# Kernel optimization log

Measured on AMD Instinct MI355X. Metric: run time of the kernel, lower is better.

Reference implementation:

```python
import jax, jax.numpy as jnp
import numpy as np

HIDDEN = 1024
HEADS = 16
HEAD_DIM = HIDDEN // HEADS
POS_DIM = 128
B, S = 2, 2048
ROPE_BASE = 10000.0


def setup_inputs() -> dict:
    key = jax.random.key(0)
    ks = jax.random.split(key, 8)
    sd = 1.0 / np.sqrt(HIDDEN)
    return {
        "x":   jax.random.normal(ks[0], (B, S, HIDDEN), dtype=jnp.float32),
        "W_q": jax.random.normal(ks[1], (HIDDEN, HIDDEN), dtype=jnp.float32) * sd,
        "W_k": jax.random.normal(ks[2], (HIDDEN, HIDDEN), dtype=jnp.float32) * sd,
        "W_v": jax.random.normal(ks[3], (HIDDEN, HIDDEN), dtype=jnp.float32) * sd,
        "W_o": jax.random.normal(ks[4], (HIDDEN, HIDDEN), dtype=jnp.float32) * sd,
        "repo_W1": jax.random.normal(ks[5], (HIDDEN, POS_DIM), dtype=jnp.float32) * sd,
        "repo_b1": jnp.zeros((POS_DIM,), dtype=jnp.float32),
        "repo_W2": jax.random.normal(ks[6], (POS_DIM, 1), dtype=jnp.float32) * (1.0 / np.sqrt(POS_DIM)),
        "repo_b2": jnp.zeros((1,), dtype=jnp.float32),
    }


def _repo_positions(x, W1, b1, W2, b2):
    # 2-layer MLP -> scalar per token; softplus + cumsum gives monotone learned positions
    h = jax.nn.gelu(jnp.einsum("bsd,dp->bsp", x, W1) + b1)
    raw = (jnp.einsum("bsp,po->bso", h, W2) + b2)[..., 0]      # (B, S)
    return jnp.cumsum(jax.nn.softplus(raw), axis=1)             # (B, S)


def _apply_rope(q, k, positions):
    # q, k: (B, S, H, Dh); positions: (B, S) continuous
    half = HEAD_DIM // 2
    inv_freq = 1.0 / (ROPE_BASE ** (jnp.arange(0, HEAD_DIM, 2, dtype=jnp.float32) / HEAD_DIM))
    angles = positions[:, :, None] * inv_freq                   # (B, S, half)
    cos = jnp.cos(angles)[:, :, None, :]                        # (B, S, 1, half)
    sin = jnp.sin(angles)[:, :, None, :]

    def rot(t):
        t1, t2 = t[..., :half], t[..., half:]
        return jnp.concatenate([t1 * cos - t2 * sin, t1 * sin + t2 * cos], axis=-1)

    return rot(q), rot(k)


def reference(x, W_q, W_k, W_v, W_o, repo_W1, repo_b1, repo_W2, repo_b2):
    scale = 1.0 / np.sqrt(HEAD_DIM)
    q = jnp.einsum("bsd,de->bse", x, W_q).reshape(B, S, HEADS, HEAD_DIM)
    k = jnp.einsum("bsd,de->bse", x, W_k).reshape(B, S, HEADS, HEAD_DIM)
    v = jnp.einsum("bsd,de->bse", x, W_v).reshape(B, S, HEADS, HEAD_DIM)

    positions = _repo_positions(x, repo_W1, repo_b1, repo_W2, repo_b2)
    q, k = _apply_rope(q, k, positions)

    # explicit O(S^2) attention, matching the torch module
    scores = jnp.einsum("bqhd,bkhd->bhqk", q, k) * scale        # (B, H, S, S)
    attn = jax.nn.softmax(scores, axis=-1)
    out = jnp.einsum("bhqk,bkhd->bqhd", attn, v)                # (B, S, H, Dh)
    out = out.reshape(B, S, HIDDEN)
    return jnp.einsum("bsd,de->bse", out, W_o)
```

## Files before the change

### kernel.cpp

```cpp
#include <hip/hip_runtime.h>
#include <hip/hip_bf16.h>
#include <math.h>

#define HIDDEN 1024
#define HEADS 16
#define HEAD_DIM 64
#define POS_DIM 128
#define BATCH 2
#define SEQ 2048
#define TOKENS (BATCH * SEQ)

typedef _Float16 f16;
typedef __attribute__((ext_vector_type(8))) _Float16 f16x8;
typedef __attribute__((ext_vector_type(4))) _Float16 f16x4;
typedef __attribute__((ext_vector_type(4))) float f32x4;

__device__ __forceinline__ void glds16(const f16* g, f16* l) {
    __builtin_amdgcn_global_load_lds((const __attribute__((address_space(1))) unsigned int*)g,
                                     (__attribute__((address_space(3))) unsigned int*)l, 16, 0, 0);
}

__global__ __launch_bounds__(256) void cast_x_kernel(const float* __restrict__ x,
                                                     f16* __restrict__ o) {
    const int i = (blockIdx.x * 256 + threadIdx.x) * 8;
    const float4 u = *(const float4*)(x + i);
    const float4 v = *(const float4*)(x + i + 4);
    f16x8 r = {(f16)u.x, (f16)u.y, (f16)u.z, (f16)u.w,
               (f16)v.x, (f16)v.y, (f16)v.z, (f16)v.w};
    *(f16x8*)(o + i) = r;
}

__global__ __launch_bounds__(256) void cast_wt4_kernel(const float* __restrict__ W0,
                                                       const float* __restrict__ W1,
                                                       const float* __restrict__ W2,
                                                       const float* __restrict__ W3,
                                                       f16* __restrict__ Wt) {
    __shared__ float ts[32][33];
    const int t = threadIdx.x;
    const int z = blockIdx.z;
    const float* W = (z == 0) ? W0 : (z == 1) ? W1 : (z == 2) ? W2 : W3;
    f16* dst = Wt + (size_t)z * HIDDEN * HIDDEN;
    const int k0 = blockIdx.y * 32, n0 = blockIdx.x * 32;
    {
        const int r = t >> 3, c4 = (t & 7) * 4;
        const float4 u = *(const float4*)(W + (size_t)(k0 + r) * HIDDEN + n0 + c4);
        ts[r][c4 + 0] = u.x; ts[r][c4 + 1] = u.y; ts[r][c4 + 2] = u.z; ts[r][c4 + 3] = u.w;
    }
    __syncthreads();
    {
        const int r = t >> 3, c4 = (t & 7) * 4;
        f16* o = dst + (size_t)(n0 + r) * HIDDEN + k0 + c4;
        o[0] = (f16)ts[c4 + 0][r]; o[1] = (f16)ts[c4 + 1][r];
        o[2] = (f16)ts[c4 + 2][r]; o[3] = (f16)ts[c4 + 3][r];
    }
}

__global__ __launch_bounds__(256) void cast_w1t_kernel(const float* __restrict__ W1,
                                                       f16* __restrict__ Wh,
                                                       f16* __restrict__ Wl) {
    __shared__ float ts[32][33];
    const int t = threadIdx.x;
    const int k0 = blockIdx.y * 32, p0 = blockIdx.x * 32;
    {
        const int r = t >> 3, c4 = (t & 7) * 4;
        const float4 u = *(const float4*)(W1 + (size_t)(k0 + r) * POS_DIM + p0 + c4);
        ts[r][c4 + 0] = u.x; ts[r][c4 + 1] = u.y; ts[r][c4 + 2] = u.z; ts[r][c4 + 3] = u.w;
    }
    __syncthreads();
    {
        const int r = t >> 3, c4 = (t & 7) * 4;
        f16* oh = Wh + (size_t)(p0 + r) * HIDDEN + k0 + c4;
        f16* ol = Wl + (size_t)(p0 + r) * HIDDEN + k0 + c4;
#pragma unroll
        for (int u = 0; u < 4; ++u) {
            const float v = ts[c4 + u][r];
            const f16 hi = (f16)v;
            oh[u] = hi;
            ol[u] = (f16)(v - (float)hi);
        }
    }
}

__global__ __launch_bounds__(256, 3) void gemm_gll(const f16* __restrict__ A,
                                                   const f16* __restrict__ Bt,
                                                   f16* __restrict__ Cb,
                                                   float* __restrict__ Cf,
                                                   int N, int f16out) {
    __shared__ __align__(16) f16 As[128 * 64];
    __shared__ __align__(16) f16 Bs[128 * 64];
    const int tid = threadIdx.x;
    const int w = tid >> 6, lane = tid & 63;
    const int g = lane >> 4, c = lane & 15;
    const int m0 = blockIdx.y * 128, n0 = blockIdx.x * 128;
    const int wm = (w & 1) * 64, wn = (w >> 1) * 64;

    const int lrow = lane >> 3;
    const int lseg = (lane & 7) ^ lrow;
    const f16* gA = A + (size_t)(m0 + w * 32 + lrow) * 1024 + lseg * 8;
    const f16* gB = Bt + (size_t)(n0 + w * 32 + lrow) * 1024 + lseg * 8;
    f16* lA = &As[(w * 32) * 64];
    f16* lB = &Bs[(w * 32) * 64];

    f32x4 acc[4][4];
    const f32x4 z = {0.f, 0.f, 0.f, 0.f};
#pragma unroll
    for (int i = 0; i < 4; ++i)
#pragma unroll
        for (int j = 0; j < 4; ++j) acc[i][j] = z;

    const int rsw = c & 7;
    for (int k0 = 0; k0 < 1024; k0 += 64) {
        __syncthreads();
#pragma unroll
        for (int p = 0; p < 4; ++p) {
            glds16(gA + (size_t)p * 8 * 1024 + k0, lA + p * 8 * 64);
            glds16(gB + (size_t)p * 8 * 1024 + k0, lB + p * 8 * 64);
        }
        __syncthreads();
#pragma unroll
        for (int s = 0; s < 2; ++s) {
            f16x8 af[4], bf[4];
#pragma unroll
            for (int i = 0; i < 4; ++i)
                af[i] = *(const f16x8*)&As[(wm + i * 16 + c) * 64 + (((s * 4 + g) ^ rsw) * 8)];
#pragma unroll
            for (int j = 0; j < 4; ++j)
                bf[j] = *(const f16x8*)&Bs[(wn + j * 16 + c) * 64 + (((s * 4 + g) ^ rsw) * 8)];
#pragma unroll
            for (int i = 0; i < 4; ++i)
#pragma unroll
                for (int j = 0; j < 4; ++j)
                    acc[i][j] = __builtin_amdgcn_mfma_f32_16x16x32_f16(af[i], bf[j], acc[i][j], 0, 0, 0);
        }
    }
#pragma unroll
    for (int i = 0; i < 4; ++i)
#pragma unroll
        for (int j = 0; j < 4; ++j)
#pragma unroll
            for (int r = 0; r < 4; ++r) {
                const size_t off = (size_t)(m0 + wm + i * 16 + 4 * g + r) * N + n0 + wn + j * 16 + c;
                if (f16out) Cb[off] = (f16)acc[i][j][r];
                else Cf[off] = acc[i][j][r];
            }
}

__device__ __forceinline__ float gelu_tanh(float x) {
    const float kA = 0.7978845608028654f;
    return 0.5f * x * (1.0f + tanhf(kA * (x + 0.044715f * x * x * x)));
}

__global__ __launch_bounds__(256, 2) void repo_mfma(const float* __restrict__ x,
                                                    const f16* __restrict__ w1h,
                                                    const f16* __restrict__ w1l,
                                                    const float* __restrict__ b1,
                                                    const float* __restrict__ W2,
                                                    const float* __restrict__ b2,
                                                    float* __restrict__ raw) {
    __shared__ __align__(16) f16 Ash[64 * 32], Asl[64 * 32];
    __shared__ __align__(16) f16 Bsh[128 * 32], Bsl[128 * 32];
    __shared__ float red[4][64];
    const int tid = threadIdx.x;
    const int w = tid >> 6, lane = tid & 63;
    const int g = lane >> 4, c = lane & 15;
    const int m0 = blockIdx.x * 64;

    const int arow = tid >> 2, aseg = tid & 3;
    const int aslot = (aseg ^ ((arow ^ (arow >> 2)) & 3)) << 3;
    const float* gA = x + (size_t)(m0 + arow) * 1024 + aseg * 8;
    const f16* gBh0 = w1h + (size_t)arow * 1024 + aseg * 8;
    const f16* gBh1 = w1h + (size_t)(arow + 64) * 1024 + aseg * 8;
    const f16* gBl0 = w1l + (size_t)arow * 1024 + aseg * 8;
    const f16* gBl1 = w1l + (size_t)(arow + 64) * 1024 + aseg * 8;
    f16* sAh = &Ash[arow * 32 + aslot];
    f16* sAl = &Asl[arow * 32 + aslot];
    f16* sBh0 = &Bsh[arow * 32 + aslot];
    f16* sBh1 = &Bsh[(arow + 64) * 32 + aslot];
    f16* sBl0 = &Bsl[arow * 32 + aslot];
    f16* sBl1 = &Bsl[(arow + 64) * 32 + aslot];

    const int foff = ((g ^ ((c ^ (c >> 2)) & 3)) << 3);

    f32x4 acc[4][2];
    const f32x4 z = {0.f, 0.f, 0.f, 0.f};
#pragma unroll
    for (int i = 0; i < 4; ++i) { acc[i][0] = z; acc[i][1] = z; }

    float4 pa0 = *(const float4*)gA;
    float4 pa1 = *(const float4*)(gA + 4);
    f16x8 pbh0 = *(const f16x8*)gBh0, pbh1 = *(const f16x8*)gBh1;
    f16x8 pbl0 = *(const f16x8*)gBl0, pbl1 = *(const f16x8*)gBl1;

    for (int k0 = 0; k0 < 1024; k0 += 32) {
        __syncthreads();
        {
            const float av[8] = {pa0.x, pa0.y, pa0.z, pa0.w, pa1.x, pa1.y, pa1.z, pa1.w};
            f16x8 ah, al;
#pragma unroll
            for (int u = 0; u < 8; ++u) {
                const f16 hi = (f16)av[u];
                ah[u] = hi;
                al[u] = (f16)(av[u] - (float)hi);
            }
            *(f16x8*)sAh = ah; *(f16x8*)sAl = al;
            *(f16x8*)sBh0 = pbh0; *(f16x8*)sBh1 = pbh1;
            *(f16x8*)sBl0 = pbl0; *(f16x8*)sBl1 = pbl1;
        }
        __syncthreads();
        if (k0 + 32 < 1024) {
            pa0 = *(const float4*)(gA + k0 + 32);
            pa1 = *(const float4*)(gA + k0 + 36);
            pbh0 = *(const f16x8*)(gBh0 + k0 + 32);
            pbh1 = *(const f16x8*)(gBh1 + k0 + 32);
            pbl0 = *(const f16x8*)(gBl0 + k0 + 32);
            pbl1 = *(const f16x8*)(gBl1 + k0 + 32);
        }
        f16x8 ah[4], al[4], bh[2], bl[2];
#pragma unroll
        for (int i = 0; i < 4; ++i) {
            ah[i] = *(const f16x8*)&Ash[(i * 16 + c) * 32 + foff];
            al[i] = *(const f16x8*)&Asl[(i * 16 + c) * 32 + foff];
        }
#pragma unroll
        for (int j = 0; j < 2; ++j) {
            bh[j] = *(const f16x8*)&Bsh[(w * 32 + j * 16 + c) * 32 + foff];
            bl[j] = *(const f16x8*)&Bsl[(w * 32 + j * 16 + c) * 32 + foff];
        }
#pragma unroll
        for (int i = 0; i < 4; ++i)
#pragma unroll
            for (int j = 0; j < 2; ++j) {
                acc[i][j] = __builtin_amdgcn_mfma_f32_16x16x32_f16(ah[i], bh[j], acc[i][j], 0, 0, 0);
                acc[i][j] = __builtin_amdgcn_mfma_f32_16x16x32_f16(ah[i], bl[j], acc[i][j], 0, 0, 0);
                acc[i][j] = __builtin_amdgcn_mfma_f32_16x16x32_f16(al[i], bh[j], acc[i][j], 0, 0, 0);
            }
    }
    float b1v[2], w2v[2];
#pragma unroll
    for (int j = 0; j < 2; ++j) {
        const int col = w * 32 + j * 16 + c;
        b1v[j] = b1[col];
        w2v[j] = W2[col];
    }
    float part[4][4];
#pragma unroll
    for (int i = 0; i < 4; ++i)
#pragma unroll
        for (int r = 0; r < 4; ++r) {
            float s = 0.f;
#pragma unroll
            for (int j = 0; j < 2; ++j)
                s += gelu_tanh(acc[i][j][r] + b1v[j]) * w2v[j];
            s += __shfl_xor(s, 1, 64);
            s += __shfl_xor(s, 2, 64);
            s += __shfl_xor(s, 4, 64);
            s += __shfl_xor(s, 8, 64);
            part[i][r] = s;
        }
    if (c == 0)
#pragma unroll
        for (int i = 0; i < 4; ++i)
#pragma unroll
            for (int r = 0; r < 4; ++r)
                red[w][i * 16 + 4 * g + r] = part[i][r];
    __syncthreads();
    if (tid < 64)
        raw[m0 + tid] = red[0][tid] + red[1][tid] + red[2][tid] + red[3][tid] + b2[0];
}

__device__ __forceinline__ double softplus_d(double x) {
    return (x > 0.0) ? x + log1p(exp(-x)) : log1p(exp(x));
}

__global__ __launch_bounds__(256) void repo_cumsum_kernel(const float* __restrict__ raw,
                                                          float* __restrict__ pos) {
    __shared__ double bufA[256];
    __shared__ double bufB[256];
    const int b = blockIdx.x;
    const int t = threadIdx.x;
    const float* r = raw + (size_t)b * SEQ;

    double loc[8];
    double sum = 0.0;
#pragma unroll
    for (int i = 0; i < 8; ++i) {
        sum += softplus_d((double)r[t * 8 + i]);
        loc[i] = sum;
    }
    bufA[t] = sum;
    __syncthreads();

    double* src = bufA;
    double* dst = bufB;
    for (int off = 1; off < 256; off <<= 1) {
        double v = src[t];
        if (t >= off) v += src[t - off];
        dst[t] = v;
        __syncthreads();
        double* tmp = src; src = dst; dst = tmp;
    }
    const double excl = src[t] - sum;
#pragma unroll
    for (int i = 0; i < 8; ++i)
        pos[(size_t)b * SEQ + t * 8 + i] = (float)(excl + loc[i]);
}

__global__ __launch_bounds__(256) void sctab_kernel(const float* __restrict__ pos,
                                                    float* __restrict__ costab,
                                                    float* __restrict__ sintab) {
    const int idx = blockIdx.x * 256 + threadIdx.x;
    const int tok = idx >> 5, i = idx & 31;
    const double ang = (double)pos[tok] * exp(-(double)i * 0.28782313662425574);
    double sa, ca;
    sincos(ang, &sa, &ca);
    costab[idx] = (float)ca;
    sintab[idx] = (float)sa;
}

__global__ __launch_bounds__(256) void packkv_kernel(f16* __restrict__ qkv,
                                                     const float* __restrict__ costab,
                                                     const float* __restrict__ sintab,
                                                     f16* __restrict__ kfo,
                                                     f16* __restrict__ vfo) {
    __shared__ __align__(16) f16 kds[64][72];
    __shared__ __align__(16) f16 vds[64][72];
    const int t = threadIdx.x;
    const int s0 = blockIdx.x * 64;
    const int h = blockIdx.y, b = blockIdx.z;
    const int key = t >> 2, part = t & 3;
    const int tok = b * SEQ + s0 + key;
    {
        float cs[8], sn[8];
        *(float4*)cs       = *(const float4*)(costab + tok * 32 + part * 8);
        *(float4*)(cs + 4) = *(const float4*)(costab + tok * 32 + part * 8 + 4);
        *(float4*)sn       = *(const float4*)(sintab + tok * 32 + part * 8);
        *(float4*)(sn + 4) = *(const float4*)(sintab + tok * 32 + part * 8 + 4);
        f16* qrow = qkv + (size_t)tok * 3072 + h * HEAD_DIM;
        {
            f16x8 lo = *(const f16x8*)(qrow + part * 8);
            f16x8 hi = *(const f16x8*)(qrow + part * 8 + 32);
#pragma unroll
            for (int u = 0; u < 8; ++u) {
                const float l = (float)lo[u], hh = (float)hi[u];
                lo[u] = (f16)(l * cs[u] - hh * sn[u]);
                hi[u] = (f16)(l * sn[u] + hh * cs[u]);
            }
            *(f16x8*)(qrow + part * 8) = lo;
            *(f16x8*)(qrow + part * 8 + 32) = hi;
        }
        const f16* krow = qrow + 1024;
        {
            f16x8 lo = *(const f16x8*)(krow + part * 8);
            f16x8 hi = *(const f16x8*)(krow + part * 8 + 32);
#pragma unroll
            for (int u = 0; u < 8; ++u) {
                const float l = (float)lo[u], hh = (float)hi[u];
                kds[key][part * 8 + u]      = (f16)(l * cs[u] - hh * sn[u]);
                kds[key][32 + part * 8 + u] = (f16)(l * sn[u] + hh * cs[u]);
            }
        }
        const f16* vrow = qrow + 2048;
        f16x8 v0 = *(const f16x8*)(vrow + part * 16);
        f16x8 v1 = *(const f16x8*)(vrow + part * 16 + 8);
#pragma unroll
        for (int u = 0; u < 8; ++u) {
            vds[part * 16 + u][key] = v0[u];
            vds[part * 16 + 8 + u][key] = v1[u];
        }
    }
    __syncthreads();
    const size_t cb = ((size_t)((b * HEADS + h) * 32) + blockIdx.x) * 4096;
#pragma unroll
    for (int p = 0; p < 2; ++p) {
        const int idx = p * 256 + t;
        const int frag = idx >> 6, lane = idx & 63;
        const int jn = frag >> 1, half = frag & 1, g = lane >> 4, c = lane & 15;
        *(f16x8*)(kfo + cb + frag * 512 + lane * 8) =
            *(const f16x8*)(&kds[jn * 16 + c][half * 32 + g * 8]);
    }
#pragma unroll
    for (int p = 0; p < 4; ++p) {
        const int idx = p * 256 + t;
        const int frag = idx >> 6, lane = idx & 63;
        const int jd = frag >> 2, jn = frag & 3, g = lane >> 4, c = lane & 15;
        *(f16x4*)(vfo + cb + frag * 256 + lane * 4) =
            *(const f16x4*)(&vds[jd * 16 + c][jn * 16 + 4 * g]);
    }
}

__global__ __launch_bounds__(256, 2) void attn_f16(const f16* __restrict__ qkv,
                                                   const f16* __restrict__ kfr,
                                                   const f16* __restrict__ vfr,
                                                   f16* __restrict__ aof0,
                                                   f16* __restrict__ aof1,
                                                   float* __restrict__ lsb) {
    __shared__ __align__(16) f16 kls[4096];
    __shared__ __align__(16) f16 vls[4096];
    __shared__ __align__(16) f16 ot[4][32][72];
    const int tid = threadIdx.x;
    const int w = tid >> 6, lane = tid & 63;
    const int g = lane >> 4, c = lane & 15;

    const int wid = blockIdx.x;
    const int xcd = wid & 7, slot = wid >> 3;
    const int combo = xcd * 8 + (slot >> 4);
    const int xblk = slot & 15;
    const int h = combo & 15;
    const int zz = combo >> 4;
    const int b = zz >> 1, half = zz & 1;

    const int bh = b * HEADS + h;
    const int row0 = xblk * 128 + w * 32;
    const int ch0 = half * 16;

    const f16* qb = qkv + (size_t)(b * SEQ + row0) * 3072 + h * HEAD_DIM + g * 8;
    const f16* kfb = kfr + (size_t)bh * 32 * 4096;
    const f16* vfb = vfr + (size_t)bh * 32 * 4096;

    f16x8 qf[2][2];
#pragma unroll
    for (int i = 0; i < 2; ++i) {
        qf[i][0] = *(const f16x8*)(qb + (size_t)(i * 16 + c) * 3072);
        qf[i][1] = *(const f16x8*)(qb + (size_t)(i * 16 + c) * 3072 + 32);
    }
    const f32x4 z = {0.f, 0.f, 0.f, 0.f};
    f32x4 acc[4][2];
    f32x4 accl[2];
#pragma unroll
    for (int jd = 0; jd < 4; ++jd) { acc[jd][0] = z; acc[jd][1] = z; }
    accl[0] = z; accl[1] = z;

    const f16x4 ones = {(f16)1.f, (f16)1.f, (f16)1.f, (f16)1.f};
    const float SC = 0.125f * 1.4426950408889634f;

    for (int cc = 0; cc < 16; ++cc) {
        const int ch = ch0 + cc;
        __syncthreads();
        {
            const f16* kg = kfb + (size_t)ch * 4096 + w * 1024 + lane * 8;
            const f16* vg = vfb + (size_t)ch * 4096 + w * 1024 + lane * 8;
            glds16(kg, kls + w * 1024);
            glds16(kg + 512, kls + w * 1024 + 512);
            glds16(vg, vls + w * 1024);
            glds16(vg + 512, vls + w * 1024 + 512);
        }
        __syncthreads();

        f16x8 kf[8];
        f16x4 vf[16];
#pragma unroll
        for (int f = 0; f < 8; ++f) kf[f] = *(const f16x8*)(kls + lane * 8 + f * 512);
#pragma unroll
        for (int f = 0; f < 16; ++f) vf[f] = *(const f16x4*)(vls + lane * 4 + f * 256);

#pragma unroll
        for (int i = 0; i < 2; ++i) {
            f32x4 s[4];
#pragma unroll
            for (int jn = 0; jn < 4; ++jn) {
                s[jn] = __builtin_amdgcn_mfma_f32_16x16x32_f16(kf[jn * 2], qf[i][0], z, 0, 0, 0);
                s[jn] = __builtin_amdgcn_mfma_f32_16x16x32_f16(kf[jn * 2 + 1], qf[i][1], s[jn], 0, 0, 0);
            }
#pragma unroll
            for (int jn = 0; jn < 4; ++jn) {
                f16x4 pf;
#pragma unroll
                for (int r = 0; r < 4; ++r)
                    pf[r] = (f16)__builtin_amdgcn_exp2f(fmaf(s[jn][r], SC, -8.0f));
                accl[i] = __builtin_amdgcn_mfma_f32_16x16x16f16(ones, pf, accl[i], 0, 0, 0);
#pragma unroll
                for (int jd = 0; jd < 4; ++jd)
                    acc[jd][i] = __builtin_amdgcn_mfma_f32_16x16x16f16(vf[jd * 4 + jn], pf, acc[jd][i], 0, 0, 0);
            }
        }
    }

    if (lane < 16) {
#pragma unroll
        for (int i = 0; i < 2; ++i)
            lsb[((size_t)(half * 32 + bh)) * SEQ + row0 + i * 16 + lane] = accl[i][0];
    }
#pragma unroll
    for (int i = 0; i < 2; ++i)
#pragma unroll
        for (int jd = 0; jd < 4; ++jd)
#pragma unroll
            for (int r = 0; r < 4; ++r)
                ot[w][i * 16 + c][jd * 16 + 4 * g + r] = (f16)acc[jd][i][r];
    f16* aofH = half ? aof1 : aof0;
    const int tr = lane >> 1, hf = lane & 1;
    f16* aob = aofH + (size_t)(b * SEQ + row0 + tr) * HIDDEN + h * HEAD_DIM + hf * 32;
#pragma unroll
    for (int q = 0; q < 4; ++q)
        *(f16x8*)(aob + q * 8) = *(const f16x8*)(&ot[w][tr][hf * 32 + q * 8]);
}

__global__ __launch_bounds__(256) void combine_kernel(f16* __restrict__ a0,
                                                      const f16* __restrict__ a1,
                                                      const float* __restrict__ lsb) {
    const int idx = blockIdx.x * 256 + threadIdx.x;
    const int part = idx & 127;
    const int tok = idx >> 7;
    const int h = part >> 3, d8 = (part & 7) * 8;
    const int b = tok >> 11, s = tok & 2047;
    const size_t li = (size_t)(b * HEADS + h) * SEQ + s;
    const float inv = 1.0f / (lsb[li] + lsb[32 * SEQ + li]);
    const size_t off = (size_t)tok * HIDDEN + h * HEAD_DIM + d8;
    const f16x8 u = *(const f16x8*)(a0 + off);
    const f16x8 v = *(const f16x8*)(a1 + off);
    f16x8 o;
#pragma unroll
    for (int q = 0; q < 8; ++q) o[q] = (f16)(((float)u[q] + (float)v[q]) * inv);
    *(f16x8*)(a0 + off) = o;
}

extern "C" void kernel_launch(void* const* d_in, const int* in_sizes, int n_in,
                              void* d_out, int out_size, void* d_ws, size_t ws_size,
                              hipStream_t stream) {
    const float* x   = (const float*)d_in[0];
    const float* W_q = (const float*)d_in[1];
    const float* W_k = (const float*)d_in[2];
    const float* W_v = (const float*)d_in[3];
    const float* W_o = (const float*)d_in[4];
    const float* rW1 = (const float*)d_in[5];
    const float* rb1 = (const float*)d_in[6];
    const float* rW2 = (const float*)d_in[7];
    const float* rb2 = (const float*)d_in[8];
    float* out = (float*)d_out;

    const size_t MAT = (size_t)TOKENS * HIDDEN;
    const size_t WSZ = (size_t)HIDDEN * HIDDEN;
    f16* x16  = (f16*)d_ws;
    f16* wqkv = x16 + MAT;
    f16* wot  = wqkv + 3 * WSZ;
    f16* qkv  = wot + WSZ;
    f16* kfr  = qkv + 3 * MAT;
    f16* vfr  = kfr + MAT;
    f16* aof0 = vfr + MAT;
    f16* aof1 = aof0 + MAT;
    f16* w1h  = aof1 + MAT;
    f16* w1l  = w1h + POS_DIM * HIDDEN;
    float* raw    = (float*)(w1l + POS_DIM * HIDDEN);
    float* pos    = raw + TOKENS;
    float* costab = pos + TOKENS;
    float* sintab = costab + TOKENS * 32;
    float* lsb    = sintab + TOKENS * 32;

    cast_x_kernel<<<MAT / 2048, 256, 0, stream>>>(x, x16);
    cast_wt4_kernel<<<dim3(32, 32, 4), 256, 0, stream>>>(W_q, W_k, W_v, W_o, wqkv);
    cast_w1t_kernel<<<dim3(4, 32), 256, 0, stream>>>(rW1, w1h, w1l);

    gemm_gll<<<dim3(24, 32), 256, 0, stream>>>(x16, wqkv, qkv, nullptr, 3072, 1);

    repo_mfma<<<64, 256, 0, stream>>>(x, w1h, w1l, rb1, rW2, rb2, raw);
    repo_cumsum_kernel<<<BATCH, 256, 0, stream>>>(raw, pos);
    sctab_kernel<<<TOKENS * 32 / 256, 256, 0, stream>>>(pos, costab, sintab);

    packkv_kernel<<<dim3(SEQ / 64, HEADS, BATCH), 256, 0, stream>>>(qkv, costab, sintab, kfr, vfr);

    attn_f16<<<dim3(1024), 256, 0, stream>>>(qkv, kfr, vfr, aof0, aof1, lsb);
    combine_kernel<<<TOKENS * 128 / 256, 256, 0, stream>>>(aof0, aof1, lsb);

    gemm_gll<<<dim3(8, 32), 256, 0, stream>>>(aof0, wot, nullptr, out, 1024, 0);
}
```

Baseline: 256.6 us.

## Use 16x16x32 MFMA for PV product via bpermute-repacked P fragments

```diff
diff --git a/kernel.cpp b/kernel.cpp
--- a/kernel.cpp
+++ b/kernel.cpp
@@ -18,6 +18,12 @@
 __device__ __forceinline__ void glds16(const f16* g, f16* l) {
     __builtin_amdgcn_global_load_lds((const __attribute__((address_space(1))) unsigned int*)g,
                                      (__attribute__((address_space(3))) unsigned int*)l, 16, 0, 0);
+}
+
+__device__ __forceinline__ unsigned pack2f16(float a, float b) {
+    union { _Float16 h[2]; unsigned u; } x;
+    x.h[0] = (f16)a; x.h[1] = (f16)b;
+    return x.u;
 }
 
 __global__ __launch_bounds__(256) void cast_x_kernel(const float* __restrict__ x,
@@ -379,12 +385,12 @@
             *(const f16x8*)(&kds[jn * 16 + c][half * 32 + g * 8]);
     }
 #pragma unroll
-    for (int p = 0; p < 4; ++p) {
+    for (int p = 0; p < 2; ++p) {
         const int idx = p * 256 + t;
         const int frag = idx >> 6, lane = idx & 63;
-        const int jd = frag >> 2, jn = frag & 3, g = lane >> 4, c = lane & 15;
-        *(f16x4*)(vfo + cb + frag * 256 + lane * 4) =
-            *(const f16x4*)(&vds[jd * 16 + c][jn * 16 + 4 * g]);
+        const int jd = frag >> 1, kk = frag & 1, g = lane >> 4, c = lane & 15;
+        *(f16x8*)(vfo + cb + frag * 512 + lane * 8) =
+            *(const f16x8*)(&vds[jd * 16 + c][kk * 32 + g * 8]);
     }
 }
 
@@ -430,8 +436,14 @@
     for (int jd = 0; jd < 4; ++jd) { acc[jd][0] = z; acc[jd][1] = z; }
     accl[0] = z; accl[1] = z;
 
-    const f16x4 ones = {(f16)1.f, (f16)1.f, (f16)1.f, (f16)1.f};
+    f16x8 ones8;
+#pragma unroll
+    for (int u = 0; u < 8; ++u) ones8[u] = (f16)1.f;
     const float SC = 0.125f * 1.4426950408889634f;
+
+    const int addrA = ((2 * (g & 1)) * 16 + c) * 4;
+    const int addrB = addrA + 64;
+    const unsigned ghi = (lane >> 5) & 1;
 
     for (int cc = 0; cc < 16; ++cc) {
         const int ch = ch0 + cc;
@@ -447,11 +459,11 @@
         __syncthreads();
 
         f16x8 kf[8];
-        f16x4 vf[16];
+        f16x8 vf[8];
 #pragma unroll
         for (int f = 0; f < 8; ++f) kf[f] = *(const f16x8*)(kls + lane * 8 + f * 512);
 #pragma unroll
-        for (int f = 0; f < 16; ++f) vf[f] = *(const f16x4*)(vls + lane * 4 + f * 256);
+        for (int f = 0; f < 8; ++f) vf[f] = *(const f16x8*)(vls + lane * 8 + f * 512);
 
 #pragma unroll
         for (int i = 0; i < 2; ++i) {
@@ -461,16 +473,37 @@
                 s[jn] = __builtin_amdgcn_mfma_f32_16x16x32_f16(kf[jn * 2], qf[i][0], z, 0, 0, 0);
                 s[jn] = __builtin_amdgcn_mfma_f32_16x16x32_f16(kf[jn * 2 + 1], qf[i][1], s[jn], 0, 0, 0);
             }
+            unsigned pk[4][2];
 #pragma unroll
             for (int jn = 0; jn < 4; ++jn) {
-                f16x4 pf;
-#pragma unroll
-                for (int r = 0; r < 4; ++r)
-                    pf[r] = (f16)__builtin_amdgcn_exp2f(fmaf(s[jn][r], SC, -8.0f));
-                accl[i] = __builtin_amdgcn_mfma_f32_16x16x16f16(ones, pf, accl[i], 0, 0, 0);
+                float e0 = __builtin_amdgcn_exp2f(fmaf(s[jn][0], SC, -8.0f));
+                float e1 = __builtin_amdgcn_exp2f(fmaf(s[jn][1], SC, -8.0f));
+                float e2 = __builtin_amdgcn_exp2f(fmaf(s[jn][2], SC, -8.0f));
+                float e3 = __builtin_amdgcn_exp2f(fmaf(s[jn][3], SC, -8.0f));
+                pk[jn][0] = pack2f16(e0, e1);
+                pk[jn][1] = pack2f16(e2, e3);
+            }
+#pragma unroll
+            for (int kk = 0; kk < 2; ++kk) {
+                const int j0 = 2 * kk, j1 = 2 * kk + 1;
+                const int b0A = __builtin_amdgcn_ds_bpermute(addrA, (int)pk[j0][0]);
+                const int b1A = __builtin_amdgcn_ds_bpermute(addrA, (int)pk[j0][1]);
+                const int b0B = __builtin_amdgcn_ds_bpermute(addrB, (int)pk[j0][0]);
+                const int b1B = __builtin_amdgcn_ds_bpermute(addrB, (int)pk[j0][1]);
+                const int c0A = __builtin_amdgcn_ds_bpermute(addrA, (int)pk[j1][0]);
+                const int c1A = __builtin_amdgcn_ds_bpermute(addrA, (int)pk[j1][1]);
+                const int c0B = __builtin_amdgcn_ds_bpermute(addrB, (int)pk[j1][0]);
+                const int c1B = __builtin_amdgcn_ds_bpermute(addrB, (int)pk[j1][1]);
+                union { unsigned u[4]; f16x8 v; } tb;
+                tb.u[0] = ghi ? (unsigned)c0A : (unsigned)b0A;
+                tb.u[1] = ghi ? (unsigned)c1A : (unsigned)b1A;
+                tb.u[2] = ghi ? (unsigned)c0B : (unsigned)b0B;
+                tb.u[3] = ghi ? (unsigned)c1B : (unsigned)b1B;
+                const f16x8 pB = tb.v;
+                accl[i] = __builtin_amdgcn_mfma_f32_16x16x32_f16(ones8, pB, accl[i], 0, 0, 0);
 #pragma unroll
                 for (int jd = 0; jd < 4; ++jd)
-                    acc[jd][i] = __builtin_amdgcn_mfma_f32_16x16x16f16(vf[jd * 4 + jn], pf, acc[jd][i], 0, 0, 0);
+                    acc[jd][i] = __builtin_amdgcn_mfma_f32_16x16x32_f16(vf[jd * 2 + kk], pB, acc[jd][i], 0, 0, 0);
             }
         }
     }
```

Result: slower. 261.7 us (+2.0%).

## Halve attention query tile per wave and compute denominator via shuffles

Applied to the files above, without the earlier changes.

```diff
diff --git a/kernel.cpp b/kernel.cpp
--- a/kernel.cpp
+++ b/kernel.cpp
@@ -396,41 +396,36 @@
                                                    float* __restrict__ lsb) {
     __shared__ __align__(16) f16 kls[4096];
     __shared__ __align__(16) f16 vls[4096];
-    __shared__ __align__(16) f16 ot[4][32][72];
+    __shared__ __align__(16) f16 ot[4][16][72];
     const int tid = threadIdx.x;
     const int w = tid >> 6, lane = tid & 63;
     const int g = lane >> 4, c = lane & 15;
 
     const int wid = blockIdx.x;
     const int xcd = wid & 7, slot = wid >> 3;
-    const int combo = xcd * 8 + (slot >> 4);
-    const int xblk = slot & 15;
+    const int combo = xcd * 8 + (slot >> 5);
+    const int xblk = slot & 31;
     const int h = combo & 15;
     const int zz = combo >> 4;
     const int b = zz >> 1, half = zz & 1;
 
     const int bh = b * HEADS + h;
-    const int row0 = xblk * 128 + w * 32;
+    const int row0 = xblk * 64 + w * 16;
     const int ch0 = half * 16;
 
     const f16* qb = qkv + (size_t)(b * SEQ + row0) * 3072 + h * HEAD_DIM + g * 8;
     const f16* kfb = kfr + (size_t)bh * 32 * 4096;
     const f16* vfb = vfr + (size_t)bh * 32 * 4096;
 
-    f16x8 qf[2][2];
-#pragma unroll
-    for (int i = 0; i < 2; ++i) {
-        qf[i][0] = *(const f16x8*)(qb + (size_t)(i * 16 + c) * 3072);
-        qf[i][1] = *(const f16x8*)(qb + (size_t)(i * 16 + c) * 3072 + 32);
-    }
+    const f16x8 qf0 = *(const f16x8*)(qb + (size_t)c * 3072);
+    const f16x8 qf1 = *(const f16x8*)(qb + (size_t)c * 3072 + 32);
+
     const f32x4 z = {0.f, 0.f, 0.f, 0.f};
-    f32x4 acc[4][2];
-    f32x4 accl[2];
-#pragma unroll
-    for (int jd = 0; jd < 4; ++jd) { acc[jd][0] = z; acc[jd][1] = z; }
-    accl[0] = z; accl[1] = z;
-
-    const f16x4 ones = {(f16)1.f, (f16)1.f, (f16)1.f, (f16)1.f};
+    f32x4 acc[4];
+#pragma unroll
+    for (int jd = 0; jd < 4; ++jd) acc[jd] = z;
+    float dloc = 0.f;
+
     const float SC = 0.125f * 1.4426950408889634f;
 
     for (int cc = 0; cc < 16; ++cc) {
@@ -453,46 +448,44 @@
 #pragma unroll
         for (int f = 0; f < 16; ++f) vf[f] = *(const f16x4*)(vls + lane * 4 + f * 256);
 
-#pragma unroll
-        for (int i = 0; i < 2; ++i) {
-            f32x4 s[4];
-#pragma unroll
-            for (int jn = 0; jn < 4; ++jn) {
-                s[jn] = __builtin_amdgcn_mfma_f32_16x16x32_f16(kf[jn * 2], qf[i][0], z, 0, 0, 0);
-                s[jn] = __builtin_amdgcn_mfma_f32_16x16x32_f16(kf[jn * 2 + 1], qf[i][1], s[jn], 0, 0, 0);
-            }
-#pragma unroll
-            for (int jn = 0; jn < 4; ++jn) {
-                f16x4 pf;
-#pragma unroll
-                for (int r = 0; r < 4; ++r)
-                    pf[r] = (f16)__builtin_amdgcn_exp2f(fmaf(s[jn][r], SC, -8.0f));
-                accl[i] = __builtin_amdgcn_mfma_f32_16x16x16f16(ones, pf, accl[i], 0, 0, 0);
-#pragma unroll
-                for (int jd = 0; jd < 4; ++jd)
-                    acc[jd][i] = __builtin_amdgcn_mfma_f32_16x16x16f16(vf[jd * 4 + jn], pf, acc[jd][i], 0, 0, 0);
-            }
-        }
-    }
-
-    if (lane < 16) {
-#pragma unroll
-        for (int i = 0; i < 2; ++i)
-            lsb[((size_t)(half * 32 + bh)) * SEQ + row0 + i * 16 + lane] = accl[i][0];
-    }
-#pragma unroll
-    for (int i = 0; i < 2; ++i)
-#pragma unroll
-        for (int jd = 0; jd < 4; ++jd)
-#pragma unroll
-            for (int r = 0; r < 4; ++r)
-                ot[w][i * 16 + c][jd * 16 + 4 * g + r] = (f16)acc[jd][i][r];
+        f32x4 s[4];
+#pragma unroll
+        for (int jn = 0; jn < 4; ++jn) {
+            s[jn] = __builtin_amdgcn_mfma_f32_16x16x32_f16(kf[jn * 2], qf0, z, 0, 0, 0);
+            s[jn] = __builtin_amdgcn_mfma_f32_16x16x32_f16(kf[jn * 2 + 1], qf1, s[jn], 0, 0, 0);
+        }
+#pragma unroll
+        for (int jn = 0; jn < 4; ++jn) {
+            const float e0 = __builtin_amdgcn_exp2f(fmaf(s[jn][0], SC, -8.0f));
+            const float e1 = __builtin_amdgcn_exp2f(fmaf(s[jn][1], SC, -8.0f));
+            const float e2 = __builtin_amdgcn_exp2f(fmaf(s[jn][2], SC, -8.0f));
+            const float e3 = __builtin_amdgcn_exp2f(fmaf(s[jn][3], SC, -8.0f));
+            dloc += (e0 + e1) + (e2 + e3);
+            f16x4 pf = {(f16)e0, (f16)e1, (f16)e2, (f16)e3};
+#pragma unroll
+            for (int jd = 0; jd < 4; ++jd)
+                acc[jd] = __builtin_amdgcn_mfma_f32_16x16x16f16(vf[jd * 4 + jn], pf, acc[jd], 0, 0, 0);
+        }
+    }
+
+    dloc += __shfl_xor(dloc, 16, 64);
+    dloc += __shfl_xor(dloc, 32, 64);
+    if (lane < 16)
+        lsb[((size_t)(half * 32 + bh)) * SEQ + row0 + lane] = dloc;
+
+#pragma unroll
+    for (int jd = 0; jd < 4; ++jd)
+#pragma unroll
+        for (int r = 0; r < 4; ++r)
+            ot[w][c][jd * 16 + 4 * g + r] = (f16)acc[jd][r];
     f16* aofH = half ? aof1 : aof0;
-    const int tr = lane >> 1, hf = lane & 1;
-    f16* aob = aofH + (size_t)(b * SEQ + row0 + tr) * HIDDEN + h * HEAD_DIM + hf * 32;
-#pragma unroll
-    for (int q = 0; q < 4; ++q)
-        *(f16x8*)(aob + q * 8) = *(const f16x8*)(&ot[w][tr][hf * 32 + q * 8]);
+#pragma unroll
+    for (int p = 0; p < 2; ++p) {
+        const int idx = p * 64 + lane;
+        const int row = idx >> 3, seg = idx & 7;
+        *(f16x8*)(aofH + (size_t)(b * SEQ + row0 + row) * HIDDEN + h * HEAD_DIM + seg * 8) =
+            *(const f16x8*)(&ot[w][row][seg * 8]);
+    }
 }
 
 __global__ __launch_bounds__(256) void combine_kernel(f16* __restrict__ a0,
@@ -558,7 +551,7 @@
 
     packkv_kernel<<<dim3(SEQ / 64, HEADS, BATCH), 256, 0, stream>>>(qkv, costab, sintab, kfr, vfr);
 
-    attn_f16<<<dim3(1024), 256, 0, stream>>>(qkv, kfr, vfr, aof0, aof1, lsb);
+    attn_f16<<<dim3(2048), 256, 0, stream>>>(qkv, kfr, vfr, aof0, aof1, lsb);
     combine_kernel<<<TOKENS * 128 / 256, 256, 0, stream>>>(aof0, aof1, lsb);
 
     gemm_gll<<<dim3(8, 32), 256, 0, stream>>>(aof0, wot, nullptr, out, 1024, 0);
```

After: 255.0 us. No clear change (-0.6%).

## Load two KV chunks per barrier and replace ones-MFMA row sum with VALU reduction

Applied to the files above, without the earlier changes.

```diff
diff --git a/kernel.cpp b/kernel.cpp
--- a/kernel.cpp
+++ b/kernel.cpp
@@ -394,9 +394,7 @@
                                                    f16* __restrict__ aof0,
                                                    f16* __restrict__ aof1,
                                                    float* __restrict__ lsb) {
-    __shared__ __align__(16) f16 kls[4096];
-    __shared__ __align__(16) f16 vls[4096];
-    __shared__ __align__(16) f16 ot[4][32][72];
+    __shared__ __align__(16) f16 smem[16384];
     const int tid = threadIdx.x;
     const int w = tid >> 6, lane = tid & 63;
     const int g = lane >> 4, c = lane & 15;
@@ -425,74 +423,91 @@
     }
     const f32x4 z = {0.f, 0.f, 0.f, 0.f};
     f32x4 acc[4][2];
-    f32x4 accl[2];
 #pragma unroll
     for (int jd = 0; jd < 4; ++jd) { acc[jd][0] = z; acc[jd][1] = z; }
-    accl[0] = z; accl[1] = z;
-
-    const f16x4 ones = {(f16)1.f, (f16)1.f, (f16)1.f, (f16)1.f};
+    float dloc[2] = {0.f, 0.f};
+
     const float SC = 0.125f * 1.4426950408889634f;
 
-    for (int cc = 0; cc < 16; ++cc) {
-        const int ch = ch0 + cc;
+    f16* kls = smem;
+    f16* vls = smem + 8192;
+
+    for (int it = 0; it < 8; ++it) {
+        const int ch = ch0 + it * 2;
         __syncthreads();
         {
             const f16* kg = kfb + (size_t)ch * 4096 + w * 1024 + lane * 8;
             const f16* vg = vfb + (size_t)ch * 4096 + w * 1024 + lane * 8;
             glds16(kg, kls + w * 1024);
             glds16(kg + 512, kls + w * 1024 + 512);
+            glds16(kg + 4096, kls + 4096 + w * 1024);
+            glds16(kg + 4096 + 512, kls + 4096 + w * 1024 + 512);
             glds16(vg, vls + w * 1024);
             glds16(vg + 512, vls + w * 1024 + 512);
-        }
-        __syncthreads();
-
-        f16x8 kf[8];
-        f16x4 vf[16];
-#pragma unroll
-        for (int f = 0; f < 8; ++f) kf[f] = *(const f16x8*)(kls + lane * 8 + f * 512);
-#pragma unroll
-        for (int f = 0; f < 16; ++f) vf[f] = *(const f16x4*)(vls + lane * 4 + f * 256);
-
-#pragma unroll
-        for (int i = 0; i < 2; ++i) {
-            f32x4 s[4];
-#pragma unroll
-            for (int jn = 0; jn < 4; ++jn) {
-                s[jn] = __builtin_amdgcn_mfma_f32_16x16x32_f16(kf[jn * 2], qf[i][0], z, 0, 0, 0);
-                s[jn] = __builtin_amdgcn_mfma_f32_16x16x32_f16(kf[jn * 2 + 1], qf[i][1], s[jn], 0, 0, 0);
+            glds16(vg + 4096, vls + 4096 + w * 1024);
+            glds16(vg + 4096 + 512, vls + 4096 + w * 1024 + 512);
+        }
+        __syncthreads();
+
+#pragma unroll
+        for (int sub = 0; sub < 2; ++sub) {
+            const f16* kbp = kls + sub * 4096;
+            const f16* vbp = vls + sub * 4096;
+            f16x8 kf[8];
+            f16x4 vf[16];
+#pragma unroll
+            for (int f = 0; f < 8; ++f) kf[f] = *(const f16x8*)(kbp + lane * 8 + f * 512);
+#pragma unroll
+            for (int f = 0; f < 16; ++f) vf[f] = *(const f16x4*)(vbp + lane * 4 + f * 256);
+
+#pragma unroll
+            for (int i = 0; i < 2; ++i) {
+                f32x4 s[4];
+#pragma unroll
+                for (int jn = 0; jn < 4; ++jn) {
+                    s[jn] = __builtin_amdgcn_mfma_f32_16x16x32_f16(kf[jn * 2], qf[i][0], z, 0, 0, 0);
+                    s[jn] = __builtin_amdgcn_mfma_f32_16x16x32_f16(kf[jn * 2 + 1], qf[i][1], s[jn], 0, 0, 0);
+                }
+#pragma unroll
+                for (int jn = 0; jn < 4; ++jn) {
+                    const float e0 = __builtin_amdgcn_exp2f(fmaf(s[jn][0], SC, -8.0f));
+                    const float e1 = __builtin_amdgcn_exp2f(fmaf(s[jn][1], SC, -8.0f));
+                    const float e2 = __builtin_amdgcn_exp2f(fmaf(s[jn][2], SC, -8.0f));
+                    const float e3 = __builtin_amdgcn_exp2f(fmaf(s[jn][3], SC, -8.0f));
+                    dloc[i] += (e0 + e1) + (e2 + e3);
+                    f16x4 pf = {(f16)e0, (f16)e1, (f16)e2, (f16)e3};
+#pragma unroll
+                    for (int jd = 0; jd < 4; ++jd)
+                        acc[jd][i] = __builtin_amdgcn_mfma_f32_16x16x16f16(vf[jd * 4 + jn], pf, acc[jd][i], 0, 0, 0);
+                }
             }
-#pragma unroll
-            for (int jn = 0; jn < 4; ++jn) {
-                f16x4 pf;
-#pragma unroll
-                for (int r = 0; r < 4; ++r)
-                    pf[r] = (f16)__builtin_amdgcn_exp2f(fmaf(s[jn][r], SC, -8.0f));
-                accl[i] = __builtin_amdgcn_mfma_f32_16x16x16f16(ones, pf, accl[i], 0, 0, 0);
-#pragma unroll
-                for (int jd = 0; jd < 4; ++jd)
-                    acc[jd][i] = __builtin_amdgcn_mfma_f32_16x16x16f16(vf[jd * 4 + jn], pf, acc[jd][i], 0, 0, 0);
-            }
-        }
-    }
-
-    if (lane < 16) {
+        }
+    }
+    __syncthreads();
+
+#pragma unroll
+    for (int i = 0; i < 2; ++i) {
+        dloc[i] += __shfl_xor(dloc[i], 16, 64);
+        dloc[i] += __shfl_xor(dloc[i], 32, 64);
+    }
+    if (lane < 16)
 #pragma unroll
         for (int i = 0; i < 2; ++i)
-            lsb[((size_t)(half * 32 + bh)) * SEQ + row0 + i * 16 + lane] = accl[i][0];
-    }
+            lsb[((size_t)(half * 32 + bh)) * SEQ + row0 + i * 16 + lane] = dloc[i];
+
 #pragma unroll
     for (int i = 0; i < 2; ++i)
 #pragma unroll
         for (int jd = 0; jd < 4; ++jd)
 #pragma unroll
             for (int r = 0; r < 4; ++r)
-                ot[w][i * 16 + c][jd * 16 + 4 * g + r] = (f16)acc[jd][i][r];
+                smem[(w * 32 + i * 16 + c) * 72 + jd * 16 + 4 * g + r] = (f16)acc[jd][i][r];
     f16* aofH = half ? aof1 : aof0;
     const int tr = lane >> 1, hf = lane & 1;
     f16* aob = aofH + (size_t)(b * SEQ + row0 + tr) * HIDDEN + h * HEAD_DIM + hf * 32;
 #pragma unroll
     for (int q = 0; q < 4; ++q)
-        *(f16x8*)(aob + q * 8) = *(const f16x8*)(&ot[w][tr][hf * 32 + q * 8]);
+        *(f16x8*)(aob + q * 8) = *(const f16x8*)(smem + (w * 32 + tr) * 72 + hf * 32 + q * 8);
 }
 
 __global__ __launch_bounds__(256) void combine_kernel(f16* __restrict__ a0,
```

After: 253.6 us. Within noise of the previous version (-1.1%).
